# Optimization experiments

Measured on AMD Instinct MI355X. Metric: run time of the kernel, lower is better.

## Reference

```python
import jax, jax.numpy as jnp
import numpy as np

TEMPERATURE = 8.0  # sqrt(d_k=64)
NEG_INF = -1.0e9   # matches masked_fill value in source


def setup_inputs() -> dict:
    key = jax.random.key(0)
    kq, kk, kv, km = jax.random.split(key, 4)
    B, H, T, C = 2, 16, 2048, 64
    q = jax.random.normal(kq, (B, H, T, C), dtype=jnp.float32)
    k = jax.random.normal(kk, (B, H, T, C), dtype=jnp.float32)
    v = jax.random.normal(kv, (B, H, T, C), dtype=jnp.float32)
    mask = jax.random.randint(km, (B, 1, T, T), 0, 2, dtype=jnp.int32)
    return {"q": q, "k": k, "v": v, "mask": mask}


def reference(q, k, v, mask):
    # attn = (q / temperature) @ k^T   -> [b, h, T, T]
    attn = jnp.einsum("bhqc,bhkc->bhqk", q / TEMPERATURE, k)
    attn = jnp.where(mask == 0, NEG_INF, attn)
    attn = jax.nn.softmax(attn, axis=-1)
    # dropout is identity in eval / deterministic reference
    output = jnp.einsum("bhqk,bhkc->bhqc", attn, v)
    return (output, attn)
```

## Files before the change

### kernel.cpp

```cpp
#include <hip/hip_runtime.h>
#include <stdint.h>
#include <stddef.h>

#define T_DIM 2048
#define C_DIM 64
#define SCALE_L2E 0.18033688011112042f
#define STG_P 40

typedef __bf16 bf16x8 __attribute__((ext_vector_type(8)));
typedef float f32x4 __attribute__((ext_vector_type(4)));
typedef unsigned int u32x4 __attribute__((ext_vector_type(4)));
typedef unsigned int u32x2 __attribute__((ext_vector_type(2)));
typedef int i32x4 __attribute__((ext_vector_type(4)));
typedef unsigned short u16t;

static __device__ __forceinline__ unsigned f2bf_bits(float f) {
  unsigned u = __builtin_bit_cast(unsigned, f);
  u += 0x7fffu + ((u >> 16) & 1u);
  return u >> 16;
}
static __device__ __forceinline__ bf16x8 asfrag(u32x4 u) {
  return __builtin_bit_cast(bf16x8, u);
}
static __device__ __forceinline__ bf16x8 pack8(f32x4 a, f32x4 b) {
  u32x4 u;
  u[0] = f2bf_bits(a[0]) | (f2bf_bits(a[1]) << 16);
  u[1] = f2bf_bits(a[2]) | (f2bf_bits(a[3]) << 16);
  u[2] = f2bf_bits(b[0]) | (f2bf_bits(b[1]) << 16);
  u[3] = f2bf_bits(b[2]) | (f2bf_bits(b[3]) << 16);
  return __builtin_bit_cast(bf16x8, u);
}
static __device__ __forceinline__ bf16x8 ld_cvt8(const float* p) {
  return pack8(*(const f32x4*)p, *(const f32x4*)(p + 4));
}
static __device__ __forceinline__ float bf_lo(unsigned u) {
  return __builtin_bit_cast(float, u << 16);
}
static __device__ __forceinline__ float bf_hi(unsigned u) {
  return __builtin_bit_cast(float, u & 0xffff0000u);
}

__global__ __launch_bounds__(256) void prep_kernel(
    const float* __restrict__ k, const float* __restrict__ v,
    const int* __restrict__ mask, u16t* __restrict__ kb,
    u16t* __restrict__ vt2, unsigned* __restrict__ mb) {
  if (blockIdx.x < 2048) {
    const size_t e0 = ((size_t)blockIdx.x * 256 + threadIdx.x) * 8;
    const float* src = k + e0;
    u32x4 u;
    f32x4 a = *(const f32x4*)src;
    f32x4 b = *(const f32x4*)(src + 4);
    u[0] = f2bf_bits(a[0]) | (f2bf_bits(a[1]) << 16);
    u[1] = f2bf_bits(a[2]) | (f2bf_bits(a[3]) << 16);
    u[2] = f2bf_bits(b[0]) | (f2bf_bits(b[1]) << 16);
    u[3] = f2bf_bits(b[2]) | (f2bf_bits(b[3]) << 16);
    *(u32x4*)(kb + e0) = u;
  } else if (blockIdx.x < 2304) {
    const int gid = (blockIdx.x - 2048) * 256 + threadIdx.x;
    const int bh = gid >> 11;
    const int j = gid & (T_DIM - 1);
    const float* src = v + ((size_t)bh * T_DIM + j) * C_DIM;
    u16t* dst = vt2 + ((size_t)bh * 64 + (j >> 5)) * 2048 + (j & 31);
#pragma unroll
    for (int c0 = 0; c0 < C_DIM; c0 += 4) {
      f32x4 x = *(const f32x4*)(src + c0);
#pragma unroll
      for (int e = 0; e < 4; ++e)
        dst[(size_t)(c0 + e) * 32] = (u16t)f2bf_bits(x[e]);
    }
  } else {
    const int gid = (blockIdx.x - 2304) * 256 + threadIdx.x;
    const int* src = mask + (size_t)gid * 32;
    unsigned bits = 0;
#pragma unroll
    for (int t = 0; t < 8; ++t) {
      i32x4 x = *(const i32x4*)(src + t * 4);
      bits |= (x[0] != 0 ? 1u : 0u) << (t * 4);
      bits |= (x[1] != 0 ? 1u : 0u) << (t * 4 + 1);
      bits |= (x[2] != 0 ? 1u : 0u) << (t * 4 + 2);
      bits |= (x[3] != 0 ? 1u : 0u) << (t * 4 + 3);
    }
    mb[gid] = bits;
  }
}

template <bool USE_PREP>
__global__ __launch_bounds__(256, 3) void attn_fwd(
    const float* __restrict__ qp, const float* __restrict__ kp,
    const float* __restrict__ vp, const int* __restrict__ maskp,
    const u16t* __restrict__ kbp, const u16t* __restrict__ vt2p,
    const unsigned* __restrict__ mbp, float* __restrict__ outp,
    float* __restrict__ attnp) {
  __shared__ float Of[4096];
  __shared__ float rowsum[64];
  __shared__ float rls[16];

  const int tid = threadIdx.x;
  const int wave = tid >> 6;
  const int lane = tid & 63;
  const int quad = lane >> 4;
  const int l15 = lane & 15;

  const int h = blockIdx.x & 15;
  const int qb = (blockIdx.x >> 4) & 127;
  const int b = blockIdx.x >> 11;
  const int bh = b * 16 + h;
  const int q0 = qb << 4;

  const float* qrow = qp + ((size_t)bh * T_DIM + q0 + l15) * C_DIM + quad * 8;
  const bf16x8 qf0 = ld_cvt8(qrow);
  const bf16x8 qf1 = ld_cvt8(qrow + 32);

  const u16t* kbbase = kbp + (size_t)bh * T_DIM * C_DIM;
  const float* kfbase = kp + (size_t)bh * T_DIM * C_DIM;
  const float* vfbase = vp + (size_t)bh * T_DIM * C_DIM;
  const u16t* vtbase = vt2p + (size_t)bh * (C_DIM * T_DIM) +
                       (size_t)wave * 16 * 2048 + l15 * 32 + quad * 8;
  const unsigned* mrowb =
      mbp + ((size_t)b * T_DIM + q0 + l15) * (T_DIM / 32) + wave * 16;
  const int* mrow = maskp + ((size_t)b * T_DIM + q0 + l15) * T_DIM;

  u16t* const stg0 = (u16t*)Of + wave * (2 * 16 * STG_P);

  f32x4 ao0 = {0.f, 0.f, 0.f, 0.f};
  f32x4 ao1 = {0.f, 0.f, 0.f, 0.f};
  f32x4 ao2 = {0.f, 0.f, 0.f, 0.f};
  f32x4 ao3 = {0.f, 0.f, 0.f, 0.f};
  u32x2 pA[16], pB[16];
  float ls0 = 0.f, ls1 = 0.f;

#pragma unroll
  for (int s = 0; s < 16; ++s) {
    const int j0 = wave * 512 + s * 32;

    bf16x8 kA0, kA1, kB0, kB1;
    u32x4 vb0, vb1, vb2, vb3;
    unsigned mq = 0;
    i32x4 mA, mB;
    if constexpr (USE_PREP) {
      const u16t* ka = kbbase + (size_t)(j0 + l15) * C_DIM + quad * 8;
      kA0 = asfrag(*(const u32x4*)(ka));
      kA1 = asfrag(*(const u32x4*)(ka + 32));
      kB0 = asfrag(*(const u32x4*)(ka + 16 * C_DIM));
      kB1 = asfrag(*(const u32x4*)(ka + 16 * C_DIM + 32));
      const u16t* tb = vtbase + (size_t)s * 2048;
      vb0 = *(const u32x4*)(tb);
      vb1 = *(const u32x4*)(tb + 512);
      vb2 = *(const u32x4*)(tb + 1024);
      vb3 = *(const u32x4*)(tb + 1536);
      mq = mrowb[s] >> (quad * 4);
    } else {
      const float* ka = kfbase + (size_t)(j0 + l15) * C_DIM + quad * 8;
      kA0 = ld_cvt8(ka);
      kA1 = ld_cvt8(ka + 32);
      kB0 = ld_cvt8(ka + 16 * C_DIM);
      kB1 = ld_cvt8(ka + 16 * C_DIM + 32);
      const float* g = vfbase + (size_t)(j0 + quad * 8) * C_DIM + l15;
      auto gather = [&](int c0) -> u32x4 {
        const float* p = g + c0;
        u32x4 r;
        r[0] = f2bf_bits(p[0]) | (f2bf_bits(p[C_DIM]) << 16);
        r[1] = f2bf_bits(p[2 * C_DIM]) | (f2bf_bits(p[3 * C_DIM]) << 16);
        r[2] = f2bf_bits(p[4 * C_DIM]) | (f2bf_bits(p[5 * C_DIM]) << 16);
        r[3] = f2bf_bits(p[6 * C_DIM]) | (f2bf_bits(p[7 * C_DIM]) << 16);
        return r;
      };
      vb0 = gather(0); vb1 = gather(16); vb2 = gather(32); vb3 = gather(48);
      mA = *(const i32x4*)(mrow + j0 + quad * 4);
      mB = *(const i32x4*)(mrow + j0 + 16 + quad * 4);
    }

    f32x4 sA = {0.f, 0.f, 0.f, 0.f};
    sA = __builtin_amdgcn_mfma_f32_16x16x32_bf16(kA0, qf0, sA, 0, 0, 0);
    sA = __builtin_amdgcn_mfma_f32_16x16x32_bf16(kA1, qf1, sA, 0, 0, 0);
    f32x4 sB = {0.f, 0.f, 0.f, 0.f};
    sB = __builtin_amdgcn_mfma_f32_16x16x32_bf16(kB0, qf0, sB, 0, 0, 0);
    sB = __builtin_amdgcn_mfma_f32_16x16x32_bf16(kB1, qf1, sB, 0, 0, 0);

    const float eA0 = __builtin_exp2f(sA[0] * SCALE_L2E);
    const float eA1 = __builtin_exp2f(sA[1] * SCALE_L2E);
    const float eA2 = __builtin_exp2f(sA[2] * SCALE_L2E);
    const float eA3 = __builtin_exp2f(sA[3] * SCALE_L2E);
    const float eB0 = __builtin_exp2f(sB[0] * SCALE_L2E);
    const float eB1 = __builtin_exp2f(sB[1] * SCALE_L2E);
    const float eB2 = __builtin_exp2f(sB[2] * SCALE_L2E);
    const float eB3 = __builtin_exp2f(sB[3] * SCALE_L2E);
    float a0, a1, a2, a3, b0, b1, b2, b3;
    if constexpr (USE_PREP) {
      a0 = (mq & 0x1u) ? eA0 : 0.f;
      a1 = (mq & 0x2u) ? eA1 : 0.f;
      a2 = (mq & 0x4u) ? eA2 : 0.f;
      a3 = (mq & 0x8u) ? eA3 : 0.f;
      b0 = (mq & 0x10000u) ? eB0 : 0.f;
      b1 = (mq & 0x20000u) ? eB1 : 0.f;
      b2 = (mq & 0x40000u) ? eB2 : 0.f;
      b3 = (mq & 0x80000u) ? eB3 : 0.f;
    } else {
      a0 = mA[0] ? eA0 : 0.f;
      a1 = mA[1] ? eA1 : 0.f;
      a2 = mA[2] ? eA2 : 0.f;
      a3 = mA[3] ? eA3 : 0.f;
      b0 = mB[0] ? eB0 : 0.f;
      b1 = mB[1] ? eB1 : 0.f;
      b2 = mB[2] ? eB2 : 0.f;
      b3 = mB[3] ? eB3 : 0.f;
    }

    u32x2 wA, wB;
    wA[0] = f2bf_bits(a0) | (f2bf_bits(a1) << 16);
    wA[1] = f2bf_bits(a2) | (f2bf_bits(a3) << 16);
    wB[0] = f2bf_bits(b0) | (f2bf_bits(b1) << 16);
    wB[1] = f2bf_bits(b2) | (f2bf_bits(b3) << 16);
    pA[s] = wA;
    pB[s] = wB;

    ls0 += (a0 + a1) + (a2 + a3);
    ls1 += (b0 + b1) + (b2 + b3);

    u16t* const stg = stg0 + (s & 1) * (16 * STG_P);
    *(u32x2*)&stg[l15 * STG_P + quad * 4] = wA;
    *(u32x2*)&stg[l15 * STG_P + quad * 4 + 16] = wB;
    const bf16x8 pa = asfrag(*(const u32x4*)&stg[l15 * STG_P + quad * 8]);
    ao0 = __builtin_amdgcn_mfma_f32_16x16x32_bf16(pa, asfrag(vb0), ao0, 0, 0, 0);
    ao1 = __builtin_amdgcn_mfma_f32_16x16x32_bf16(pa, asfrag(vb1), ao1, 0, 0, 0);
    ao2 = __builtin_amdgcn_mfma_f32_16x16x32_bf16(pa, asfrag(vb2), ao2, 0, 0, 0);
    ao3 = __builtin_amdgcn_mfma_f32_16x16x32_bf16(pa, asfrag(vb3), ao3, 0, 0, 0);
  }

  float lsum = ls0 + ls1;
  lsum += __shfl_xor(lsum, 16, 64);
  lsum += __shfl_xor(lsum, 32, 64);
  if (quad == 0) rowsum[wave * 16 + l15] = lsum;
  __syncthreads();
  if (tid < 16)
    rls[tid] = 1.0f / (rowsum[tid] + rowsum[16 + tid] + rowsum[32 + tid] +
                       rowsum[48 + tid]);
  __syncthreads();
  const float rl = rls[l15];

  float* const arow =
      attnp + ((size_t)bh * T_DIM + q0 + l15) * T_DIM + quad * 4;
#pragma unroll
  for (int s = 0; s < 16; ++s) {
    const int j0 = wave * 512 + s * 32;
    const u32x2 wA = pA[s], wB = pB[s];
    f32x4 oA, oB;
    oA[0] = bf_lo(wA[0]) * rl;
    oA[1] = bf_hi(wA[0]) * rl;
    oA[2] = bf_lo(wA[1]) * rl;
    oA[3] = bf_hi(wA[1]) * rl;
    oB[0] = bf_lo(wB[0]) * rl;
    oB[1] = bf_hi(wB[0]) * rl;
    oB[2] = bf_lo(wB[1]) * rl;
    oB[3] = bf_hi(wB[1]) * rl;
    *(f32x4*)(arow + j0) = oA;
    *(f32x4*)(arow + j0 + 16) = oB;
  }

#pragma unroll
  for (int r = 0; r < 4; ++r) {
    const int qq = quad * 4 + r;
    float* dst = Of + wave * 1024 + qq * 64 + l15;
    dst[0] = ao0[r];
    dst[16] = ao1[r];
    dst[32] = ao2[r];
    dst[48] = ao3[r];
  }
  __syncthreads();
  {
    const int tq = tid >> 4;
    const int c = (tid & 15) * 4;
    f32x4 os = *(const f32x4*)&Of[tq * 64 + c];
    os += *(const f32x4*)&Of[1024 + tq * 64 + c];
    os += *(const f32x4*)&Of[2048 + tq * 64 + c];
    os += *(const f32x4*)&Of[3072 + tq * 64 + c];
    os *= rls[tq];
    *(f32x4*)(outp + ((size_t)bh * T_DIM + q0 + tq) * C_DIM + c) = os;
  }
}

extern "C" void kernel_launch(void* const* d_in, const int* in_sizes, int n_in,
                              void* d_out, int out_size, void* d_ws, size_t ws_size,
                              hipStream_t stream) {
  const float* q = (const float*)d_in[0];
  const float* k = (const float*)d_in[1];
  const float* v = (const float*)d_in[2];
  const int* mask = (const int*)d_in[3];
  float* out = (float*)d_out;
  float* attn = out + (size_t)2 * 16 * T_DIM * C_DIM;

  const size_t n_elems = (size_t)2 * 16 * T_DIM * C_DIM;
  const size_t n_mwords = (size_t)2 * T_DIM * (T_DIM / 32);
  const size_t prep_bytes = 2 * n_elems * sizeof(u16t) + n_mwords * 4;
  if (ws_size >= prep_bytes) {
    u16t* kb = (u16t*)d_ws;
    u16t* vt2 = kb + n_elems;
    unsigned* mb = (unsigned*)(vt2 + n_elems);
    prep_kernel<<<3328, 256, 0, stream>>>(k, v, mask, kb, vt2, mb);
    attn_fwd<true><<<4096, 256, 0, stream>>>(q, k, v, mask, kb, vt2, mb, out, attn);
  } else {
    attn_fwd<false><<<4096, 256, 0, stream>>>(q, k, v, mask, nullptr, nullptr,
                                              nullptr, out, attn);
  }
}
```

Measured before the change: 879.2 us.

## Coalesce attn stores via LDS restaging and tile V transpose in prep

```diff
diff --git a/kernel.cpp b/kernel.cpp
--- a/kernel.cpp
+++ b/kernel.cpp
@@ -55,21 +55,36 @@
     u[2] = f2bf_bits(b[0]) | (f2bf_bits(b[1]) << 16);
     u[3] = f2bf_bits(b[2]) | (f2bf_bits(b[3]) << 16);
     *(u32x4*)(kb + e0) = u;
-  } else if (blockIdx.x < 2304) {
-    const int gid = (blockIdx.x - 2048) * 256 + threadIdx.x;
-    const int bh = gid >> 11;
-    const int j = gid & (T_DIM - 1);
-    const float* src = v + ((size_t)bh * T_DIM + j) * C_DIM;
-    u16t* dst = vt2 + ((size_t)bh * 64 + (j >> 5)) * 2048 + (j & 31);
-#pragma unroll
-    for (int c0 = 0; c0 < C_DIM; c0 += 4) {
-      f32x4 x = *(const f32x4*)(src + c0);
-#pragma unroll
-      for (int e = 0; e < 4; ++e)
-        dst[(size_t)(c0 + e) * 32] = (u16t)f2bf_bits(x[e]);
-    }
+  } else if (blockIdx.x < 4096) {
+    __shared__ float tile[32][66];
+    const int t = threadIdx.x;
+    const int tl = blockIdx.x - 2048;
+    const int bh = tl >> 6;
+    const int t32 = tl & 63;
+    const float* src = v + ((size_t)bh * T_DIM + t32 * 32) * C_DIM;
+#pragma unroll
+    for (int u = 0; u < 2; ++u) {
+      const int vec = t + u * 256;
+      const int jj = vec >> 4;
+      const int c4 = (vec & 15) * 4;
+      const f32x4 x = *(const f32x4*)(src + jj * C_DIM + c4);
+      tile[jj][c4] = x[0];
+      tile[jj][c4 + 1] = x[1];
+      tile[jj][c4 + 2] = x[2];
+      tile[jj][c4 + 3] = x[3];
+    }
+    __syncthreads();
+    const int c = t >> 2;
+    const int j8 = (t & 3) * 8;
+    u32x4 o;
+#pragma unroll
+    for (int i = 0; i < 4; ++i) {
+      o[i] = f2bf_bits(tile[j8 + 2 * i][c]) |
+             (f2bf_bits(tile[j8 + 2 * i + 1][c]) << 16);
+    }
+    *(u32x4*)(vt2 + ((size_t)bh * 64 + t32) * 2048 + (size_t)t * 8) = o;
   } else {
-    const int gid = (blockIdx.x - 2304) * 256 + threadIdx.x;
+    const int gid = (blockIdx.x - 4096) * 256 + threadIdx.x;
     const int* src = mask + (size_t)gid * 32;
     unsigned bits = 0;
 #pragma unroll
@@ -92,6 +107,7 @@
     const unsigned* __restrict__ mbp, float* __restrict__ outp,
     float* __restrict__ attnp) {
   __shared__ float Of[4096];
+  __shared__ u16t stg[4][2][16 * STG_P];
   __shared__ float rowsum[64];
   __shared__ float rls[16];
 
@@ -119,8 +135,6 @@
   const unsigned* mrowb =
       mbp + ((size_t)b * T_DIM + q0 + l15) * (T_DIM / 32) + wave * 16;
   const int* mrow = maskp + ((size_t)b * T_DIM + q0 + l15) * T_DIM;
-
-  u16t* const stg0 = (u16t*)Of + wave * (2 * 16 * STG_P);
 
   f32x4 ao0 = {0.f, 0.f, 0.f, 0.f};
   f32x4 ao1 = {0.f, 0.f, 0.f, 0.f};
@@ -217,10 +231,10 @@
     ls0 += (a0 + a1) + (a2 + a3);
     ls1 += (b0 + b1) + (b2 + b3);
 
-    u16t* const stg = stg0 + (s & 1) * (16 * STG_P);
-    *(u32x2*)&stg[l15 * STG_P + quad * 4] = wA;
-    *(u32x2*)&stg[l15 * STG_P + quad * 4 + 16] = wB;
-    const bf16x8 pa = asfrag(*(const u32x4*)&stg[l15 * STG_P + quad * 8]);
+    u16t* const sb = stg[wave][s & 1];
+    *(u32x2*)&sb[l15 * STG_P + quad * 4] = wA;
+    *(u32x2*)&sb[l15 * STG_P + quad * 4 + 16] = wB;
+    const bf16x8 pa = asfrag(*(const u32x4*)&sb[l15 * STG_P + quad * 8]);
     ao0 = __builtin_amdgcn_mfma_f32_16x16x32_bf16(pa, asfrag(vb0), ao0, 0, 0, 0);
     ao1 = __builtin_amdgcn_mfma_f32_16x16x32_bf16(pa, asfrag(vb1), ao1, 0, 0, 0);
     ao2 = __builtin_amdgcn_mfma_f32_16x16x32_bf16(pa, asfrag(vb2), ao2, 0, 0, 0);
@@ -236,25 +250,33 @@
     rls[tid] = 1.0f / (rowsum[tid] + rowsum[16 + tid] + rowsum[32 + tid] +
                        rowsum[48 + tid]);
   __syncthreads();
-  const float rl = rls[l15];
-
-  float* const arow =
-      attnp + ((size_t)bh * T_DIM + q0 + l15) * T_DIM + quad * 4;
+
+  const int brow = lane >> 3;
+  const int bcol = (lane & 7) * 4;
+  const float rlLo = rls[brow];
+  const float rlHi = rls[8 + brow];
+  float* const arowLo =
+      attnp + ((size_t)bh * T_DIM + q0 + brow) * T_DIM + bcol;
+  float* const arowHi = arowLo + (size_t)8 * T_DIM;
 #pragma unroll
   for (int s = 0; s < 16; ++s) {
     const int j0 = wave * 512 + s * 32;
-    const u32x2 wA = pA[s], wB = pB[s];
-    f32x4 oA, oB;
-    oA[0] = bf_lo(wA[0]) * rl;
-    oA[1] = bf_hi(wA[0]) * rl;
-    oA[2] = bf_lo(wA[1]) * rl;
-    oA[3] = bf_hi(wA[1]) * rl;
-    oB[0] = bf_lo(wB[0]) * rl;
-    oB[1] = bf_hi(wB[0]) * rl;
-    oB[2] = bf_lo(wB[1]) * rl;
-    oB[3] = bf_hi(wB[1]) * rl;
-    *(f32x4*)(arow + j0) = oA;
-    *(f32x4*)(arow + j0 + 16) = oB;
+    u16t* const sb = stg[wave][s & 1];
+    *(u32x2*)&sb[l15 * STG_P + quad * 4] = pA[s];
+    *(u32x2*)&sb[l15 * STG_P + quad * 4 + 16] = pB[s];
+    const u32x2 dlo = *(const u32x2*)&sb[brow * STG_P + bcol];
+    const u32x2 dhi = *(const u32x2*)&sb[(8 + brow) * STG_P + bcol];
+    f32x4 olo, ohi;
+    olo[0] = bf_lo(dlo[0]) * rlLo;
+    olo[1] = bf_hi(dlo[0]) * rlLo;
+    olo[2] = bf_lo(dlo[1]) * rlLo;
+    olo[3] = bf_hi(dlo[1]) * rlLo;
+    ohi[0] = bf_lo(dhi[0]) * rlHi;
+    ohi[1] = bf_hi(dhi[0]) * rlHi;
+    ohi[2] = bf_lo(dhi[1]) * rlHi;
+    ohi[3] = bf_hi(dhi[1]) * rlHi;
+    *(f32x4*)(arowLo + j0) = olo;
+    *(f32x4*)(arowHi + j0) = ohi;
   }
 
 #pragma unroll
@@ -296,7 +318,7 @@
     u16t* kb = (u16t*)d_ws;
     u16t* vt2 = kb + n_elems;
     unsigned* mb = (unsigned*)(vt2 + n_elems);
-    prep_kernel<<<3328, 256, 0, stream>>>(k, v, mask, kb, vt2, mb);
+    prep_kernel<<<5120, 256, 0, stream>>>(k, v, mask, kb, vt2, mb);
     attn_fwd<true><<<4096, 256, 0, stream>>>(q, k, v, mask, kb, vt2, mb, out, attn);
   } else {
     attn_fwd<false><<<4096, 256, 0, stream>>>(q, k, v, mask, nullptr, nullptr,
```

Measured after the change: 768.5 us. 1.14x faster.
